# Kernel optimization log

Hardware: AMD Instinct MI355X
Metric: run time of the kernel (lower is better)

Reference implementation:

```python
import jax, jax.numpy as jnp
import numpy as np

B, S, H = 2, 2048, 2048
NH, NKV = 16, 4
HD = H // NH           # 128
THETA = 1000000.0


def setup_inputs() -> dict:
    key = jax.random.key(0)
    ks = jax.random.split(key, 6)
    s = 0.02
    hidden_states = jax.random.normal(ks[0], (B, S, H), jnp.float32)
    # additive causal mask, broadcast over batch and heads
    causal = jnp.tril(jnp.ones((S, S), bool))
    attention_mask = jnp.where(causal, 0.0, -1e9).astype(jnp.float32)[None, None]
    position_ids = jnp.broadcast_to(jnp.arange(S, dtype=jnp.int32), (B, S))
    wq = jax.random.normal(ks[1], (H, H), jnp.float32) * s
    bq = jnp.zeros((H,), jnp.float32)
    wk = jax.random.normal(ks[2], (H, NKV * HD), jnp.float32) * s
    bk = jnp.zeros((NKV * HD,), jnp.float32)
    wv = jax.random.normal(ks[3], (H, NKV * HD), jnp.float32) * s
    bv = jnp.zeros((NKV * HD,), jnp.float32)
    wo = jax.random.normal(ks[4], (H, H), jnp.float32) * s
    return {"hidden_states": hidden_states, "attention_mask": attention_mask,
            "position_ids": position_ids, "wq": wq, "bq": bq, "wk": wk, "bk": bk,
            "wv": wv, "bv": bv, "wo": wo}


def _rope(x, cos, sin):
    # x: [B,S,h,HD]; interleaved-pair rotation == complex multiply in original
    x2 = x.reshape(*x.shape[:-1], HD // 2, 2)
    x0, x1 = x2[..., 0], x2[..., 1]
    r0 = x0 * cos - x1 * sin
    r1 = x0 * sin + x1 * cos
    return jnp.stack([r0, r1], axis=-1).reshape(x.shape).astype(jnp.float32)


def reference(hidden_states, attention_mask, position_ids, wq, bq, wk, bk, wv, bv, wo):
    bf = jnp.bfloat16
    x = hidden_states.astype(bf)
    # projections in bf16, as flax Dense(dtype=bfloat16)
    q = (x @ wq.astype(bf) + bq.astype(bf)).reshape(B, S, NH, HD)
    k = (x @ wk.astype(bf) + bk.astype(bf)).reshape(B, S, NKV, HD)
    v = (x @ wv.astype(bf) + bv.astype(bf)).reshape(B, S, NKV, HD)
    # RoPE: freqs_cis = exp(1j * pos * inv_freq); real rotation form, identical math
    pos = position_ids[0].astype(jnp.float32)                       # [S]
    inv = 1.0 / (THETA ** (jnp.arange(0, HD, 2, dtype=jnp.float32) / HD))  # [HD/2]
    ang = pos[:, None] * inv[None, :]                               # [S, HD/2]
    cos = jnp.cos(ang)[None, :, None, :]
    sin = jnp.sin(ang)[None, :, None, :]
    q = _rope(q, cos, sin)   # cast to float32 per module dtype
    k = _rope(k, cos, sin)
    cache_k, cache_v = k, v.astype(jnp.float32)
    rep = NH // NKV
    kr = jnp.repeat(k, rep, axis=2)                                 # [B,S,NH,HD]
    vr = jnp.repeat(v, rep, axis=2).astype(jnp.float32)
    scale = 1.0 / np.sqrt(HD).astype(np.float32)
    scores = jnp.einsum('bqhd,bkhd->bhqk', q, kr) * scale + attention_mask
    # float64 cast in original is a no-op w/o x64; softmax runs in float32
    probs = jnp.clip(jax.nn.softmax(scores, axis=-1), 1e-9, 1.0 - 1e-9)
    attn = jnp.einsum('bhqk,bkhd->bqhd', probs, vr).reshape(B, S, H)
    out = attn.astype(bf) @ wo.astype(bf)   # o_proj, no bias, bf16
    return out, (cache_k, cache_v)
```

## Files before the change

### kernel.cpp

```cpp
#include <hip/hip_runtime.h>
#include <hip/hip_bf16.h>
#include <math.h>

#define B_    2
#define S_    2048
#define H_    2048
#define NH_   16
#define NKV_  4
#define HD_   128
#define M_    (B_*S_)
#define NKVH_ (NKV_*HD_)
#define QKVN  3072
#define PSTR  72

typedef __bf16 bf16x8 __attribute__((ext_vector_type(8)));
typedef __bf16 bf16x4 __attribute__((ext_vector_type(4)));
typedef float  f32x4  __attribute__((ext_vector_type(4)));

__device__ __forceinline__ float bf2f(unsigned short u){
  unsigned int i = ((unsigned int)u) << 16; float f;
  __builtin_memcpy(&f, &i, 4); return f;
}
__device__ __forceinline__ unsigned short f2bf(float f){
  unsigned int i; __builtin_memcpy(&i, &f, 4);
  unsigned int r = (i + 0x7fffu + ((i >> 16) & 1u)) >> 16;
  return (unsigned short)r;
}
__device__ __forceinline__ float fast_exp2(float x){
  float r; asm("v_exp_f32 %0, %1" : "=v"(r) : "v"(x)); return r;
}

#define GLOAD_LDS16(g, l) __builtin_amdgcn_global_load_lds( \
    (const __attribute__((address_space(1))) void*)(g), \
    (__attribute__((address_space(3))) void*)(l), 16, 0, 0)

__global__ void k_f32_to_bf16(const float* __restrict__ in, unsigned short* __restrict__ out, int n4){
  int idx = blockIdx.x * blockDim.x + threadIdx.x;
  if (idx >= n4) return;
  float4 v = reinterpret_cast<const float4*>(in)[idx];
  ushort4 o; o.x = f2bf(v.x); o.y = f2bf(v.y); o.z = f2bf(v.z); o.w = f2bf(v.w);
  reinterpret_cast<ushort4*>(out)[idx] = o;
}

__global__ void k_transpose_w(const float* __restrict__ W, unsigned short* __restrict__ Wt, int K, int N){
  __shared__ unsigned short tile[32][36];
  int t = threadIdx.x;
  int k0 = blockIdx.x * 32, n0 = blockIdx.y * 32;
  int kr = t >> 3, nc = (t & 7) * 4;
  float4 v = *reinterpret_cast<const float4*>(&W[(size_t)(k0 + kr) * N + n0 + nc]);
  tile[kr][nc+0] = f2bf(v.x); tile[kr][nc+1] = f2bf(v.y);
  tile[kr][nc+2] = f2bf(v.z); tile[kr][nc+3] = f2bf(v.w);
  __syncthreads();
  int nr = t >> 3, kc = (t & 7) * 4;
  ushort4 o;
  o.x = tile[kc+0][nr]; o.y = tile[kc+1][nr]; o.z = tile[kc+2][nr]; o.w = tile[kc+3][nr];
  *reinterpret_cast<ushort4*>(&Wt[(size_t)(n0 + nr) * K + k0 + kc]) = o;
}

__global__ void k_bias_cat(const float* __restrict__ bq, const float* __restrict__ bk,
                           const float* __restrict__ bv, float* __restrict__ out){
  int i = blockIdx.x * 256 + threadIdx.x;
  if (i >= QKVN) return;
  out[i] = (i < H_) ? bq[i] : (i < H_ + NKVH_ ? bk[i - H_] : bv[i - H_ - NKVH_]);
}

__global__ void k_rope_table(const int* __restrict__ pos, float2* __restrict__ tab){
  int idx = blockIdx.x * blockDim.x + threadIdx.x;
  if (idx >= S_ * 64) return;
  int s = idx >> 6, i = idx & 63;
  float p = (float)pos[s];
  float inv = expf(-(float)i * (13.815510557964274f / 64.0f));
  float ang = p * inv;
  tab[idx] = make_float2(cosf(ang), sinf(ang));
}

__global__ void k_rope_k(unsigned short* __restrict__ QKV, const float2* __restrict__ tab,
                         float* __restrict__ cacheK){
  int idx = blockIdx.x * blockDim.x + threadIdx.x;
  int row = idx >> 7;
  int col0 = (idx & 127) * 4;
  int s = row & (S_ - 1);
  int i0 = (col0 & (HD_ - 1)) >> 1;
  unsigned short* p = QKV + (size_t)row * QKVN + H_ + col0;
  ushort4 v = *reinterpret_cast<ushort4*>(p);
  float2 t0 = tab[(s << 6) + i0], t1 = tab[(s << 6) + i0 + 1];
  float x0 = bf2f(v.x), x1 = bf2f(v.y), x2 = bf2f(v.z), x3 = bf2f(v.w);
  float r0 = x0 * t0.x - x1 * t0.y;
  float r1 = x0 * t0.y + x1 * t0.x;
  float r2 = x2 * t1.x - x3 * t1.y;
  float r3 = x2 * t1.y + x3 * t1.x;
  ushort4 o; o.x = f2bf(r0); o.y = f2bf(r1); o.z = f2bf(r2); o.w = f2bf(r3);
  *reinterpret_cast<ushort4*>(p) = o;
  float4 c; c.x = r0; c.y = r1; c.z = r2; c.w = r3;
  reinterpret_cast<float4*>(cacheK)[idx] = c;
}

__global__ void k_transpose_v(const unsigned short* __restrict__ QKV, unsigned short* __restrict__ Vt,
                              float* __restrict__ cacheV){
  __shared__ unsigned short tile[32][36];
  int t = threadIdx.x;
  int s0 = blockIdx.x * 32, c0 = blockIdx.y * 32, b = blockIdx.z;
  int sr = t >> 3, cc = (t & 7) * 4;
  ushort4 v = *reinterpret_cast<const ushort4*>(
      &QKV[(size_t)(b * S_ + s0 + sr) * QKVN + H_ + NKVH_ + c0 + cc]);
  tile[sr][cc+0] = v.x; tile[sr][cc+1] = v.y; tile[sr][cc+2] = v.z; tile[sr][cc+3] = v.w;
  float4 cf; cf.x = bf2f(v.x); cf.y = bf2f(v.y); cf.z = bf2f(v.z); cf.w = bf2f(v.w);
  *reinterpret_cast<float4*>(&cacheV[(size_t)(b * S_ + s0 + sr) * NKVH_ + c0 + cc]) = cf;
  __syncthreads();
  int cr = t >> 3, sc = (t & 7) * 4;
  ushort4 o;
  o.x = tile[sc+0][cr]; o.y = tile[sc+1][cr]; o.z = tile[sc+2][cr]; o.w = tile[sc+3][cr];
  *reinterpret_cast<ushort4*>(&Vt[(size_t)(b * NKVH_ + c0 + cr) * S_ + s0 + sc]) = o;
}

__global__ __launch_bounds__(256, 2) void k_gemm128(
    const unsigned short* __restrict__ A,
    const unsigned short* __restrict__ Bt,
    const float* __restrict__ bias,
    unsigned short* __restrict__ Cb,
    float* __restrict__ Cf,
    int M, int N, int K)
{
  __shared__ unsigned short As[2][128 * 64];
  __shared__ unsigned short Bs[2][128 * 64];
  const int nbn = N >> 7;
  const int nwg = gridDim.x;
  int bid = blockIdx.x;
  if ((nwg & 7) == 0) bid = (bid & 7) * (nwg >> 3) + (bid >> 3);
  const int bm = bid / nbn, bn = bid % nbn;
  const int tid = threadIdx.x, lane = tid & 63, wave = tid >> 6;
  const int wr = wave >> 1, wc = wave & 1;
  const int gm0 = bm << 7, gn0 = bn << 7;
  const int l15 = lane & 15, lhi = lane >> 4;
  const int srow8 = lane >> 3;
  const int sch   = (lane & 7) ^ srow8;

  f32x4 acc[4][4];
  f32x4 zero = {0.f, 0.f, 0.f, 0.f};
  #pragma unroll
  for (int m = 0; m < 4; m++)
    #pragma unroll
    for (int n = 0; n < 4; n++) acc[m][n] = zero;

  const int nt = K >> 6;

  auto STAGE_P = [&](int kt, int bi, int p){
    int seg = p * 4 + wave;
    int row = seg * 8 + srow8;
    GLOAD_LDS16(A  + (size_t)(gm0 + row) * K + kt * 64 + sch * 8,
                &As[bi][seg * 512]);
    GLOAD_LDS16(Bt + (size_t)(gn0 + row) * K + kt * 64 + sch * 8,
                &Bs[bi][seg * 512]);
  };

  #pragma unroll
  for (int p = 0; p < 4; p++) STAGE_P(0, 0, p);
  __syncthreads();

  for (int kt = 0; kt < nt; ++kt) {
    const int cur = kt & 1, nxt = cur ^ 1;
    const bool pre = (kt + 1 < nt);

    bf16x8 bfr[4][2];
    #pragma unroll
    for (int nf = 0; nf < 4; nf++) {
      int row = wc * 64 + nf * 16 + l15;
      #pragma unroll
      for (int kk = 0; kk < 2; kk++)
        bfr[nf][kk] = *reinterpret_cast<const bf16x8*>(
            &Bs[cur][row * 64 + (((kk << 2) + lhi) ^ (row & 7)) * 8]);
    }

    #pragma unroll
    for (int mf = 0; mf < 4; mf++) {
      if (pre) STAGE_P(kt + 1, nxt, mf);
      bf16x8 af[2];
      int row = wr * 64 + mf * 16 + l15;
      #pragma unroll
      for (int kk = 0; kk < 2; kk++)
        af[kk] = *reinterpret_cast<const bf16x8*>(
            &As[cur][row * 64 + (((kk << 2) + lhi) ^ (row & 7)) * 8]);
      __builtin_amdgcn_s_setprio(1);
      #pragma unroll
      for (int nf = 0; nf < 4; nf++)
        #pragma unroll
        for (int kk = 0; kk < 2; kk++)
          acc[mf][nf] = __builtin_amdgcn_mfma_f32_16x16x32_bf16(
              af[kk], bfr[nf][kk], acc[mf][nf], 0, 0, 0);
      __builtin_amdgcn_s_setprio(0);
    }
    __syncthreads();
  }

  #pragma unroll
  for (int mf = 0; mf < 4; mf++) {
    #pragma unroll
    for (int nf = 0; nf < 4; nf++) {
      int col = gn0 + wc * 64 + nf * 16 + l15;
      float bv = bias ? bias[col] : 0.0f;
      #pragma unroll
      for (int r = 0; r < 4; r++) {
        int row = gm0 + wr * 64 + mf * 16 + lhi * 4 + r;
        size_t idx = (size_t)row * N + col;
        float v = acc[mf][nf][r] + bv;
        if (Cf) Cf[idx] = bf2f(f2bf(v));
        else    Cb[idx] = f2bf(v);
      }
    }
  }
}

__device__ __forceinline__ bf16x8 rope8(ushort4 a, ushort4 b, const float2* __restrict__ tb, float mul){
  unsigned short u[8];
  float2 c;
  c = tb[0]; { float x0=bf2f(a.x), x1=bf2f(a.y); u[0]=f2bf((x0*c.x-x1*c.y)*mul); u[1]=f2bf((x0*c.y+x1*c.x)*mul); }
  c = tb[1]; { float x0=bf2f(a.z), x1=bf2f(a.w); u[2]=f2bf((x0*c.x-x1*c.y)*mul); u[3]=f2bf((x0*c.y+x1*c.x)*mul); }
  c = tb[2]; { float x0=bf2f(b.x), x1=bf2f(b.y); u[4]=f2bf((x0*c.x-x1*c.y)*mul); u[5]=f2bf((x0*c.y+x1*c.x)*mul); }
  c = tb[3]; { float x0=bf2f(b.z), x1=bf2f(b.w); u[6]=f2bf((x0*c.x-x1*c.y)*mul); u[7]=f2bf((x0*c.y+x1*c.x)*mul); }
  bf16x8 r; __builtin_memcpy(&r, u, 16); return r;
}

__global__ __launch_bounds__(256, 2) void k_attn(
    const unsigned short* __restrict__ QKV,
    const unsigned short* __restrict__ Vt,
    const float2* __restrict__ tab,
    unsigned short* __restrict__ O)
{
  __shared__ unsigned short Ks[2][64 * 128];
  __shared__ unsigned short Vs[128 * 64];
  __shared__ unsigned short Plds[4][32 * PSTR];
  const int qb = blockIdx.x;
  const int h = blockIdx.y, b = blockIdx.z;
  const int tid = threadIdx.x, lane = tid & 63, wave = tid >> 6;
  const int l15 = lane & 15, lhi = lane >> 4;
  const int q0a = qb * 64 + wave * 16;
  const int q0b = (31 - qb) * 64 + wave * 16;
  const int kvh = h >> 2;
  const float scale = 0.08838834764831845f;
  const float LOG2E = 1.4426950408889634f;
  const float SHIFT2 = 23.083120654223414f;

  const unsigned short* Kg = QKV + (size_t)(b * S_) * QKVN + H_ + kvh * HD_;
  const unsigned short* Vg = Vt + (size_t)(b * NKV_ + kvh) * HD_ * S_;

  bf16x8 qfa[4], qfb[4];
  {
    const unsigned short* qa = QKV + (size_t)(b * S_ + q0a + l15) * QKVN + h * HD_ + lhi * 8;
    const unsigned short* qbp = QKV + (size_t)(b * S_ + q0b + l15) * QKVN + h * HD_ + lhi * 8;
    const float2* ta = tab + (size_t)(q0a + l15) * 64;
    const float2* tb = tab + (size_t)(q0b + l15) * 64;
    #pragma unroll
    for (int t = 0; t < 4; t++) {
      int i0 = t * 16 + lhi * 4;
      ushort4 a0 = *reinterpret_cast<const ushort4*>(qa + t * 32);
      ushort4 a1 = *reinterpret_cast<const ushort4*>(qa + t * 32 + 4);
      ushort4 b0 = *reinterpret_cast<const ushort4*>(qbp + t * 32);
      ushort4 b1 = *reinterpret_cast<const ushort4*>(qbp + t * 32 + 4);
      qfa[t] = rope8(a0, a1, ta + i0, scale);
      qfb[t] = rope8(b0, b1, tb + i0, scale);
    }
  }

  f32x4 oa[8], ob[8];
  f32x4 zero = {0.f, 0.f, 0.f, 0.f};
  #pragma unroll
  for (int d = 0; d < 8; d++) { oa[d] = zero; ob[d] = zero; }
  float la = 0.f, lb = 0.f;

  unsigned short* pl = &Plds[wave][0];
  const int ktmax = 31 - qb;
  const int krow = tid >> 4, kch = tid & 15;
  const int vrow = tid >> 3, vch = tid & 7;

  auto STAGE_K = [&](int kt, int bi){
    #pragma unroll
    for (int p = 0; p < 4; p++) {
      int r = p * 16 + krow;
      int cs = kch ^ (r & 7);
      GLOAD_LDS16(Kg + (size_t)(kt * 64 + r) * QKVN + cs * 8, &Ks[bi][(p * 16 + 4 * wave) * 128]);
    }
  };
  auto STAGE_V = [&](int kt){
    #pragma unroll
    for (int p = 0; p < 4; p++) {
      int r = p * 32 + vrow;
      int cs = vch ^ (r & 7);
      GLOAD_LDS16(Vg + (size_t)r * S_ + kt * 64 + cs * 8, &Vs[(p * 32 + 8 * wave) * 64]);
    }
  };

  STAGE_K(0, 0);
  __syncthreads();
  int cur = 0;

  for (int kt = 0; kt <= ktmax; ++kt) {
    STAGE_V(kt);
    if (kt < ktmax) STAGE_K(kt + 1, cur ^ 1);
    const bool doA = (kt <= qb);

    f32x4 sca[4], scb[4];
    #pragma unroll
    for (int c = 0; c < 4; c++) { sca[c] = zero; scb[c] = zero; }
    __builtin_amdgcn_s_setprio(1);
    #pragma unroll
    for (int c = 0; c < 4; c++) {
      int rk = c * 16 + l15;
      #pragma unroll
      for (int t = 0; t < 4; t++) {
        bf16x8 kf = *reinterpret_cast<const bf16x8*>(
            &Ks[cur][rk * 128 + (((t << 2) + lhi) ^ (rk & 7)) * 8]);
        scb[c] = __builtin_amdgcn_mfma_f32_16x16x32_bf16(kf, qfb[t], scb[c], 0, 0, 0);
        if (doA) sca[c] = __builtin_amdgcn_mfma_f32_16x16x32_bf16(kf, qfa[t], sca[c], 0, 0, 0);
      }
    }
    __builtin_amdgcn_s_setprio(0);

    {
      int qiB = q0b + l15;
      float acc = 0.f;
      #pragma unroll
      for (int c = 0; c < 4; c++) {
        float pv[4];
        #pragma unroll
        for (int r = 0; r < 4; r++) {
          int key = kt * 64 + c * 16 + lhi * 4 + r;
          float sv = (key > qiB) ? -1e30f : scb[c][r];
          pv[r] = fast_exp2(fmaf(sv, LOG2E, -SHIFT2));
          acc += pv[r];
        }
        bf16x4 w;
        w[0] = (__bf16)pv[0]; w[1] = (__bf16)pv[1]; w[2] = (__bf16)pv[2]; w[3] = (__bf16)pv[3];
        *reinterpret_cast<bf16x4*>(&pl[(16 + l15) * PSTR + c * 16 + lhi * 4]) = w;
      }
      lb += acc;
    }
    if (doA) {
      int qiA = q0a + l15;
      float acc = 0.f;
      #pragma unroll
      for (int c = 0; c < 4; c++) {
        float pv[4];
        #pragma unroll
        for (int r = 0; r < 4; r++) {
          int key = kt * 64 + c * 16 + lhi * 4 + r;
          float sv = (key > qiA) ? -1e30f : sca[c][r];
          pv[r] = fast_exp2(fmaf(sv, LOG2E, -SHIFT2));
          acc += pv[r];
        }
        bf16x4 w;
        w[0] = (__bf16)pv[0]; w[1] = (__bf16)pv[1]; w[2] = (__bf16)pv[2]; w[3] = (__bf16)pv[3];
        *reinterpret_cast<bf16x4*>(&pl[l15 * PSTR + c * 16 + lhi * 4]) = w;
      }
      la += acc;
    }
    asm volatile("" ::: "memory");
    bf16x8 pfb0 = *reinterpret_cast<const bf16x8*>(&pl[(16 + l15) * PSTR + lhi * 8]);
    bf16x8 pfb1 = *reinterpret_cast<const bf16x8*>(&pl[(16 + l15) * PSTR + 32 + lhi * 8]);
    bf16x8 pfa0 = pfb0, pfa1 = pfb1;
    if (doA) {
      pfa0 = *reinterpret_cast<const bf16x8*>(&pl[l15 * PSTR + lhi * 8]);
      pfa1 = *reinterpret_cast<const bf16x8*>(&pl[l15 * PSTR + 32 + lhi * 8]);
    }
    asm volatile("" ::: "memory");

    __syncthreads();

    __builtin_amdgcn_s_setprio(1);
    #pragma unroll
    for (int d = 0; d < 8; d++) {
      int rv = d * 16 + l15;
      bf16x8 vf0 = *reinterpret_cast<const bf16x8*>(&Vs[rv * 64 + (lhi ^ (rv & 7)) * 8]);
      bf16x8 vf1 = *reinterpret_cast<const bf16x8*>(&Vs[rv * 64 + ((4 + lhi) ^ (rv & 7)) * 8]);
      ob[d] = __builtin_amdgcn_mfma_f32_16x16x32_bf16(pfb0, vf0, ob[d], 0, 0, 0);
      ob[d] = __builtin_amdgcn_mfma_f32_16x16x32_bf16(pfb1, vf1, ob[d], 0, 0, 0);
      if (doA) {
        oa[d] = __builtin_amdgcn_mfma_f32_16x16x32_bf16(pfa0, vf0, oa[d], 0, 0, 0);
        oa[d] = __builtin_amdgcn_mfma_f32_16x16x32_bf16(pfa1, vf1, oa[d], 0, 0, 0);
      }
    }
    __builtin_amdgcn_s_setprio(0);

    __syncthreads();
    cur ^= 1;
  }

  la += __shfl_xor(la, 16); la += __shfl_xor(la, 32);
  lb += __shfl_xor(lb, 16); lb += __shfl_xor(lb, 32);

  #pragma unroll
  for (int r = 0; r < 4; r++) {
    int src = (lane & 48) | (lhi * 4 + r);
    float invA = 1.0f / __shfl(la, src);
    float invB = 1.0f / __shfl(lb, src);
    size_t offA = (size_t)(b * S_ + q0a + lhi * 4 + r) * H_ + h * HD_;
    size_t offB = (size_t)(b * S_ + q0b + lhi * 4 + r) * H_ + h * HD_;
    #pragma unroll
    for (int d = 0; d < 8; d++) {
      O[offA + d * 16 + l15] = f2bf(oa[d][r] * invA);
      O[offB + d * 16 + l15] = f2bf(ob[d][r] * invB);
    }
  }
}

extern "C" void kernel_launch(void* const* d_in, const int* in_sizes, int n_in,
                              void* d_out, int out_size, void* d_ws, size_t ws_size,
                              hipStream_t stream) {
  const float* hidden = (const float*)d_in[0];
  const int*   pos    = (const int*)d_in[2];
  const float* wq     = (const float*)d_in[3];
  const float* bq     = (const float*)d_in[4];
  const float* wk     = (const float*)d_in[5];
  const float* bk     = (const float*)d_in[6];
  const float* wv     = (const float*)d_in[7];
  const float* bv     = (const float*)d_in[8];
  const float* wo     = (const float*)d_in[9];

  float* outF   = (float*)d_out;
  float* cacheK = outF + (size_t)M_ * H_;
  float* cacheV = cacheK + (size_t)M_ * NKVH_;

  char* w = (char*)d_ws;
  unsigned short* Xbf  = (unsigned short*)w; w += (size_t)M_ * H_ * 2;
  unsigned short* WqT  = (unsigned short*)w; w += (size_t)H_ * H_ * 2;
  unsigned short* WkT  = (unsigned short*)w; w += (size_t)NKVH_ * H_ * 2;
  unsigned short* WvT  = (unsigned short*)w; w += (size_t)NKVH_ * H_ * 2;
  unsigned short* WoT  = (unsigned short*)w; w += (size_t)H_ * H_ * 2;
  unsigned short* QKVw = (unsigned short*)w; w += (size_t)M_ * QKVN * 2;
  unsigned short* Vt   = (unsigned short*)w; w += (size_t)M_ * NKVH_ * 2;
  float2*         tab  = (float2*)w;         w += (size_t)S_ * 64 * sizeof(float2);
  float*       biasQKV = (float*)w;          w += QKVN * sizeof(float);
  unsigned short* Ao   = Xbf;

  k_f32_to_bf16<<<(M_ * H_ / 4) / 256, 256, 0, stream>>>(hidden, Xbf, M_ * H_ / 4);
  k_transpose_w<<<dim3(64, 64), 256, 0, stream>>>(wq, WqT, H_, H_);
  k_transpose_w<<<dim3(64, 16), 256, 0, stream>>>(wk, WkT, H_, NKVH_);
  k_transpose_w<<<dim3(64, 16), 256, 0, stream>>>(wv, WvT, H_, NKVH_);
  k_transpose_w<<<dim3(64, 64), 256, 0, stream>>>(wo, WoT, H_, H_);
  k_rope_table<<<(S_ * 64) / 256, 256, 0, stream>>>(pos, tab);
  k_bias_cat<<<(QKVN + 255) / 256, 256, 0, stream>>>(bq, bk, bv, biasQKV);
  k_gemm128<<<(M_ >> 7) * (QKVN >> 7), 256, 0, stream>>>(Xbf, WqT, biasQKV, QKVw, nullptr, M_, QKVN, H_);
  k_rope_k<<<(M_ * NKVH_ / 4) / 256, 256, 0, stream>>>(QKVw, tab, cacheK);
  k_transpose_v<<<dim3(S_ / 32, NKVH_ / 32, B_), 256, 0, stream>>>(QKVw, Vt, cacheV);
  k_attn<<<dim3(16, NH_, B_), 256, 0, stream>>>(QKVw, Vt, tab, Ao);
  k_gemm128<<<(M_ >> 7) * (H_ >> 7), 256, 0, stream>>>(Ao, WoT, nullptr, nullptr, outF, M_, H_, H_);
}
```

Measured before the change: 225.1 us.

## Make GEMM waves load private LDS tiles to drop block barriers

Restructures the 128x128 GEMM so each wave stages its own 64-row A and B slices into a private LDS region. This removes all __syncthreads from the K loop, replacing them with per-wave vmcnt/lgkmcnt waits, and issues the next tile's global-to-LDS loads after the current fragments are read into registers. The cost is global and LDS traffic per block doubling (each A/B row is loaded by two waves instead of shared). The shared tile is also single-buffered per wave, so load latency is hidden only behind the MFMA block.

```diff
diff --git a/kernel.cpp b/kernel.cpp
--- a/kernel.cpp
+++ b/kernel.cpp
@@ -113,7 +113,7 @@
   *reinterpret_cast<ushort4*>(&Vt[(size_t)(b * NKVH_ + c0 + cr) * S_ + s0 + sc]) = o;
 }
 
-__global__ __launch_bounds__(256, 2) void k_gemm128(
+__global__ __launch_bounds__(256, 2) void k_gemm_wp(
     const unsigned short* __restrict__ A,
     const unsigned short* __restrict__ Bt,
     const float* __restrict__ bias,
@@ -121,8 +121,7 @@
     float* __restrict__ Cf,
     int M, int N, int K)
 {
-  __shared__ unsigned short As[2][128 * 64];
-  __shared__ unsigned short Bs[2][128 * 64];
+  __shared__ unsigned short buf[4][8192];
   const int nbn = N >> 7;
   const int nwg = gridDim.x;
   int bid = blockIdx.x;
@@ -135,6 +134,11 @@
   const int srow8 = lane >> 3;
   const int sch   = (lane & 7) ^ srow8;
 
+  unsigned short* Aw = &buf[wave][0];
+  unsigned short* Bw = &buf[wave][4096];
+  const unsigned short* Ag = A  + (size_t)(gm0 + wr * 64) * K;
+  const unsigned short* Bg = Bt + (size_t)(gn0 + wc * 64) * K;
+
   f32x4 acc[4][4];
   f32x4 zero = {0.f, 0.f, 0.f, 0.f};
   #pragma unroll
@@ -144,52 +148,42 @@
 
   const int nt = K >> 6;
 
-  auto STAGE_P = [&](int kt, int bi, int p){
-    int seg = p * 4 + wave;
-    int row = seg * 8 + srow8;
-    GLOAD_LDS16(A  + (size_t)(gm0 + row) * K + kt * 64 + sch * 8,
-                &As[bi][seg * 512]);
-    GLOAD_LDS16(Bt + (size_t)(gn0 + row) * K + kt * 64 + sch * 8,
-                &Bs[bi][seg * 512]);
+  auto STAGE = [&](int kt){
+    #pragma unroll
+    for (int i = 0; i < 8; i++) {
+      GLOAD_LDS16(Ag + (size_t)(i * 8 + srow8) * K + kt * 64 + sch * 8, Aw + i * 512);
+      GLOAD_LDS16(Bg + (size_t)(i * 8 + srow8) * K + kt * 64 + sch * 8, Bw + i * 512);
+    }
   };
 
-  #pragma unroll
-  for (int p = 0; p < 4; p++) STAGE_P(0, 0, p);
-  __syncthreads();
+  STAGE(0);
 
   for (int kt = 0; kt < nt; ++kt) {
-    const int cur = kt & 1, nxt = cur ^ 1;
-    const bool pre = (kt + 1 < nt);
-
-    bf16x8 bfr[4][2];
-    #pragma unroll
-    for (int nf = 0; nf < 4; nf++) {
-      int row = wc * 64 + nf * 16 + l15;
-      #pragma unroll
-      for (int kk = 0; kk < 2; kk++)
-        bfr[nf][kk] = *reinterpret_cast<const bf16x8*>(
-            &Bs[cur][row * 64 + (((kk << 2) + lhi) ^ (row & 7)) * 8]);
-    }
-
-    #pragma unroll
-    for (int mf = 0; mf < 4; mf++) {
-      if (pre) STAGE_P(kt + 1, nxt, mf);
-      bf16x8 af[2];
-      int row = wr * 64 + mf * 16 + l15;
-      #pragma unroll
-      for (int kk = 0; kk < 2; kk++)
-        af[kk] = *reinterpret_cast<const bf16x8*>(
-            &As[cur][row * 64 + (((kk << 2) + lhi) ^ (row & 7)) * 8]);
-      __builtin_amdgcn_s_setprio(1);
+    asm volatile("s_waitcnt vmcnt(0)" ::: "memory");
+    bf16x8 af[4][2], bfr[4][2];
+    #pragma unroll
+    for (int f = 0; f < 4; f++) {
+      int lr = f * 16 + l15;
+      #pragma unroll
+      for (int kk = 0; kk < 2; kk++) {
+        af[f][kk]  = *reinterpret_cast<const bf16x8*>(&Aw[lr * 64 + (((kk << 2) + lhi) ^ (lr & 7)) * 8]);
+        bfr[f][kk] = *reinterpret_cast<const bf16x8*>(&Bw[lr * 64 + (((kk << 2) + lhi) ^ (lr & 7)) * 8]);
+      }
+    }
+    asm volatile("s_waitcnt lgkmcnt(0)" ::: "memory");
+    __builtin_amdgcn_sched_barrier(0);
+    if (kt + 1 < nt) STAGE(kt + 1);
+
+    __builtin_amdgcn_s_setprio(1);
+    #pragma unroll
+    for (int mf = 0; mf < 4; mf++)
       #pragma unroll
       for (int nf = 0; nf < 4; nf++)
         #pragma unroll
         for (int kk = 0; kk < 2; kk++)
           acc[mf][nf] = __builtin_amdgcn_mfma_f32_16x16x32_bf16(
-              af[kk], bfr[nf][kk], acc[mf][nf], 0, 0, 0);
-      __builtin_amdgcn_s_setprio(0);
-    }
-    __syncthreads();
+              af[mf][kk], bfr[nf][kk], acc[mf][nf], 0, 0, 0);
+    __builtin_amdgcn_s_setprio(0);
   }
 
   #pragma unroll
@@ -438,9 +432,9 @@
   k_transpose_w<<<dim3(64, 64), 256, 0, stream>>>(wo, WoT, H_, H_);
   k_rope_table<<<(S_ * 64) / 256, 256, 0, stream>>>(pos, tab);
   k_bias_cat<<<(QKVN + 255) / 256, 256, 0, stream>>>(bq, bk, bv, biasQKV);
-  k_gemm128<<<(M_ >> 7) * (QKVN >> 7), 256, 0, stream>>>(Xbf, WqT, biasQKV, QKVw, nullptr, M_, QKVN, H_);
+  k_gemm_wp<<<(M_ >> 7) * (QKVN >> 7), 256, 0, stream>>>(Xbf, WqT, biasQKV, QKVw, nullptr, M_, QKVN, H_);
   k_rope_k<<<(M_ * NKVH_ / 4) / 256, 256, 0, stream>>>(QKVw, tab, cacheK);
   k_transpose_v<<<dim3(S_ / 32, NKVH_ / 32, B_), 256, 0, stream>>>(QKVw, Vt, cacheV);
   k_attn<<<dim3(16, NH_, B_), 256, 0, stream>>>(QKVw, Vt, tab, Ao);
-  k_gemm128<<<(M_ >> 7) * (H_ >> 7), 256, 0, stream>>>(Ao, WoT, nullptr, nullptr, outF, M_, H_, H_);
-}
+  k_gemm_wp<<<(M_ >> 7) * (H_ >> 7), 256, 0, stream>>>(Ao, WoT, nullptr, nullptr, outF, M_, H_, H_);
+}
```

New measurement: 231.3 us. 2.8% more time.
